# Optimization experiments

Hardware: AMD Instinct MI355X
Metric: run time of the kernel (lower is better)

Reference implementation:

```python
import jax, jax.numpy as jnp
import numpy as np

B, S, D_IN, D_OUT = 8, 2048, 4096, 4096
R, NUM_LABELERS = 32, 5
LORA_SCALING = 16 / 32  # lora_alpha / lora_r


def setup_inputs() -> dict:
    key = jax.random.key(0)
    k1, k2, k3, k4, k5, k6 = jax.random.split(key, 6)
    inp = {
        "input": jax.random.normal(k1, (B, S, D_IN), dtype=jnp.float32),
        "weight": jax.random.normal(k2, (D_OUT, D_IN), dtype=jnp.float32) * 0.02,
        "bias": jax.random.normal(k3, (D_OUT,), dtype=jnp.float32) * 0.02,
        "lora_A": jax.random.normal(k4, (NUM_LABELERS, D_IN, R), dtype=jnp.float32) * 0.02,
        "lora_B": jax.random.normal(k5, (D_OUT, R), dtype=jnp.float32) * 0.02,  # nn.Linear(r, out) weight
        "labeler_index": jax.random.randint(k6, (B,), 0, NUM_LABELERS, dtype=jnp.int64)
        if jax.config.jax_enable_x64 else jax.random.randint(k6, (B,), 0, NUM_LABELERS, dtype=jnp.int32),
    }
    return inp


def reference(input, weight, bias, lora_A, lora_B, labeler_index):
    # Base linear: F.linear(input, weight, bias) = input @ weight.T + bias
    base = jnp.einsum("bsi,oi->bso", input, weight) + bias
    # Gather per-labeler A matrices: [B, D_IN, R]
    labelers_A = lora_A[labeler_index]
    # Low-rank path: (x @ A_b) @ B.T, dropout is Identity (p=0)
    ax = jnp.einsum("bsi,bir->bsr", input, labelers_A)       # [B, S, R]
    delta = jnp.einsum("bsr,or->bso", ax, lora_B)            # [B, S, D_OUT]
    return base + delta * LORA_SCALING
```

## Files before the change

kernel.cpp:

```cpp
#include <hip/hip_runtime.h>
#include <hip/hip_bf16.h>


typedef __bf16 bf16_t;
typedef bf16_t bf16x4 __attribute__((ext_vector_type(4)));
typedef bf16_t bf16x8 __attribute__((ext_vector_type(8)));
typedef float f32x4 __attribute__((ext_vector_type(4)));

#define S_    2048
#define DIN   4096
#define DOUT  4096
#define R_    32
#define M_TOT 16384
#define KSPLIT 8

__device__ __forceinline__ void async_cp16(const bf16_t* g, bf16_t* l) {
  __builtin_amdgcn_global_load_lds((const __attribute__((address_space(1))) void*)g,
                                   (__attribute__((address_space(3))) void*)l,
                                   16, 0, 0);
}

__global__ void cast_f32_to_bf16(const float* __restrict__ src,
                                 bf16_t* __restrict__ dst, int n4) {
  int i = blockIdx.x * blockDim.x + threadIdx.x;
  if (i >= n4) return;
  f32x4 v = ((const f32x4*)src)[i];
  bf16x4 o = { (bf16_t)v[0], (bf16_t)v[1], (bf16_t)v[2], (bf16_t)v[3] };
  ((bf16x4*)dst)[i] = o;
}

__global__ __launch_bounds__(256) void transpose_loraA(
    const float* __restrict__ A, bf16_t* __restrict__ At) {
  __shared__ float tile[64][33];
  const int l = blockIdx.x / (DIN / 64);
  const int k0 = (blockIdx.x % (DIN / 64)) * 64;
  const int tid = threadIdx.x;
  {
    const int r = tid & 31, kb = tid >> 5;
#pragma unroll
    for (int p = 0; p < 8; ++p) {
      int k = p * 8 + kb;
      tile[k][r] = A[(size_t)l * DIN * R_ + (size_t)(k0 + k) * R_ + r];
    }
  }
  __syncthreads();
  {
    const int k = tid & 63, rb = tid >> 6;
#pragma unroll
    for (int p = 0; p < 8; ++p) {
      int r = p * 4 + rb;
      At[(size_t)l * R_ * DIN + (size_t)r * DIN + k0 + k] = (bf16_t)tile[k][r];
    }
  }
}

__global__ __launch_bounds__(256) void ax_partial(
    const bf16_t* __restrict__ Xb, const bf16_t* __restrict__ At,
    const int* __restrict__ lab_idx, float* __restrict__ axp) {
  __shared__ bf16_t As[128 * 64];
  __shared__ bf16_t Bs[32 * 64];
  const int tid = threadIdx.x, lane = tid & 63, wv = tid >> 6;
  const int m0 = blockIdx.x * 128;
  const int kbase = blockIdx.y * (DIN / KSPLIT);
  const int lab = lab_idx[m0 / S_];
  const bf16_t* Bsrc = At + (size_t)lab * R_ * DIN;

  f32x4 acc[2][2];
#pragma unroll
  for (int i = 0; i < 2; ++i)
#pragma unroll
    for (int j = 0; j < 2; ++j) acc[i][j] = (f32x4){0.f, 0.f, 0.f, 0.f};

  for (int kt = 0; kt < (DIN / KSPLIT) / 64; ++kt) {
    const int k0 = kbase + kt * 64;
    __syncthreads();
    {
      const int kk = (lane & 7) * 8;
#pragma unroll
      for (int j = 0; j < 4; ++j) {
        int row = j * 32 + wv * 8 + (lane >> 3);
        async_cp16(Xb + (size_t)(m0 + row) * DIN + k0 + kk,
                   As + j * 2048 + wv * 512);
      }
      int row = wv * 8 + (lane >> 3);
      async_cp16(Bsrc + (size_t)row * DIN + k0 + kk, Bs + wv * 512);
    }
    __syncthreads();
#pragma unroll
    for (int ks = 0; ks < 2; ++ks) {
      bf16x8 a[2], b[2];
#pragma unroll
      for (int mt = 0; mt < 2; ++mt)
        a[mt] = *(const bf16x8*)&As[(wv * 32 + mt * 16 + (lane & 15)) * 64 +
                                    ks * 32 + (lane >> 4) * 8];
#pragma unroll
      for (int nt = 0; nt < 2; ++nt)
        b[nt] = *(const bf16x8*)&Bs[(nt * 16 + (lane & 15)) * 64 +
                                    ks * 32 + (lane >> 4) * 8];
#pragma unroll
      for (int mt = 0; mt < 2; ++mt)
#pragma unroll
        for (int nt = 0; nt < 2; ++nt)
          acc[mt][nt] = __builtin_amdgcn_mfma_f32_16x16x32_bf16(
              a[mt], b[nt], acc[mt][nt], 0, 0, 0);
    }
  }
  float* dst = axp + (size_t)blockIdx.y * M_TOT * R_;
#pragma unroll
  for (int mt = 0; mt < 2; ++mt)
#pragma unroll
    for (int nt = 0; nt < 2; ++nt)
#pragma unroll
      for (int r = 0; r < 4; ++r) {
        int m = m0 + wv * 32 + mt * 16 + (lane >> 4) * 4 + r;
        int n = nt * 16 + (lane & 15);
        dst[(size_t)m * R_ + n] = acc[mt][nt][r];
      }
}

__global__ void ax_reduce(const float* __restrict__ axp,
                          bf16_t* __restrict__ axb, int n4) {
  int i = blockIdx.x * blockDim.x + threadIdx.x;
  if (i >= n4) return;
  f32x4 s = (f32x4){0.f, 0.f, 0.f, 0.f};
#pragma unroll
  for (int ks = 0; ks < KSPLIT; ++ks)
    s += ((const f32x4*)(axp + (size_t)ks * M_TOT * R_))[i];
  bf16x4 o = { (bf16_t)(0.5f * s[0]), (bf16_t)(0.5f * s[1]),
               (bf16_t)(0.5f * s[2]), (bf16_t)(0.5f * s[3]) };
  ((bf16x4*)axb)[i] = o;
}

__global__ __launch_bounds__(256) void main_gemm(
    const bf16_t* __restrict__ Xb, const bf16_t* __restrict__ Wb,
    const bf16_t* __restrict__ axb, const bf16_t* __restrict__ Bb,
    const float* __restrict__ bias, float* __restrict__ out) {
  __shared__ bf16_t As[128 * 32];
  __shared__ bf16_t Bs[128 * 32];
  const int tid = threadIdx.x, lane = tid & 63, wv = tid >> 6;
  const int wr = wv & 1, wc = wv >> 1;
  const int m0 = blockIdx.y * 128, n0 = blockIdx.x * 128;

  const int srow = wv * 16 + (lane >> 2);
  const int skk = (lane & 3) * 8;
  const bf16_t* pa0 = Xb + (size_t)(m0 + srow) * DIN + skk;
  const bf16_t* pa1 = pa0 + (size_t)64 * DIN;
  const bf16_t* pb0 = Wb + (size_t)(n0 + srow) * DIN + skk;
  const bf16_t* pb1 = pb0 + (size_t)64 * DIN;
  bf16_t* lA0 = As + wv * 512;
  bf16_t* lA1 = As + 2048 + wv * 512;
  bf16_t* lB0 = Bs + wv * 512;
  bf16_t* lB1 = Bs + 2048 + wv * 512;

  int offA[4], offB[4];
#pragma unroll
  for (int t = 0; t < 4; ++t) {
    offA[t] = (wr * 64 + t * 16 + (lane & 15)) * 32 + (lane >> 4) * 8;
    offB[t] = (wc * 64 + t * 16 + (lane & 15)) * 32 + (lane >> 4) * 8;
  }

  f32x4 acc[4][4];
#pragma unroll
  for (int i = 0; i < 4; ++i)
#pragma unroll
    for (int j = 0; j < 4; ++j) acc[i][j] = (f32x4){0.f, 0.f, 0.f, 0.f};

  for (int kt = 0; kt < 128; ++kt) {
    __syncthreads();
    async_cp16(pa0, lA0);
    async_cp16(pa1, lA1);
    async_cp16(pb0, lB0);
    async_cp16(pb1, lB1);
    pa0 += 32; pa1 += 32; pb0 += 32; pb1 += 32;
    __syncthreads();
    bf16x8 a[4], b[4];
#pragma unroll
    for (int t = 0; t < 4; ++t) {
      a[t] = *(const bf16x8*)&As[offA[t]];
      b[t] = *(const bf16x8*)&Bs[offB[t]];
    }
#pragma unroll
    for (int mt = 0; mt < 4; ++mt)
#pragma unroll
      for (int nt = 0; nt < 4; ++nt)
        acc[mt][nt] = __builtin_amdgcn_mfma_f32_16x16x32_bf16(
            a[mt], b[nt], acc[mt][nt], 0, 0, 0);
  }
  __syncthreads();
  async_cp16(axb + (size_t)(m0 + srow) * R_ + skk, lA0);
  async_cp16(axb + (size_t)(m0 + 64 + srow) * R_ + skk, lA1);
  async_cp16(Bb + (size_t)(n0 + srow) * R_ + skk, lB0);
  async_cp16(Bb + (size_t)(n0 + 64 + srow) * R_ + skk, lB1);
  __syncthreads();
  {
    bf16x8 a[4], b[4];
#pragma unroll
    for (int t = 0; t < 4; ++t) {
      a[t] = *(const bf16x8*)&As[offA[t]];
      b[t] = *(const bf16x8*)&Bs[offB[t]];
    }
#pragma unroll
    for (int mt = 0; mt < 4; ++mt)
#pragma unroll
      for (int nt = 0; nt < 4; ++nt)
        acc[mt][nt] = __builtin_amdgcn_mfma_f32_16x16x32_bf16(
            a[mt], b[nt], acc[mt][nt], 0, 0, 0);
  }
#pragma unroll
  for (int nt = 0; nt < 4; ++nt) {
    int n = n0 + wc * 64 + nt * 16 + (lane & 15);
    float bv = bias[n];
#pragma unroll
    for (int mt = 0; mt < 4; ++mt) {
      int m = m0 + wr * 64 + mt * 16 + (lane >> 4) * 4;
#pragma unroll
      for (int r = 0; r < 4; ++r)
        out[(size_t)(m + r) * DOUT + n] = acc[mt][nt][r] + bv;
    }
  }
}

extern "C" void kernel_launch(void* const* d_in, const int* in_sizes, int n_in,
                              void* d_out, int out_size, void* d_ws, size_t ws_size,
                              hipStream_t stream) {
  const float* X      = (const float*)d_in[0];
  const float* W      = (const float*)d_in[1];
  const float* bias   = (const float*)d_in[2];
  const float* lora_A = (const float*)d_in[3];
  const float* lora_B = (const float*)d_in[4];
  const int*   lab    = (const int*)d_in[5];
  float* out = (float*)d_out;

  char* ws = (char*)d_ws;
  bf16_t* Xb  = (bf16_t*)(ws);
  bf16_t* Wb  = (bf16_t*)(ws + 134217728UL);
  bf16_t* At  = (bf16_t*)(ws + 167772160UL);
  bf16_t* Bb  = (bf16_t*)(ws + 169082880UL);
  bf16_t* axb = (bf16_t*)(ws + 169345024UL);
  float*  axp = (float*)(ws + 170393600UL);

  cast_f32_to_bf16<<<65536, 256, 0, stream>>>(X, Xb, (M_TOT * DIN) / 4);
  cast_f32_to_bf16<<<16384, 256, 0, stream>>>(W, Wb, (DOUT * DIN) / 4);
  cast_f32_to_bf16<<<128, 256, 0, stream>>>(lora_B, Bb, (DOUT * R_) / 4);
  transpose_loraA<<<5 * (DIN / 64), 256, 0, stream>>>(lora_A, At);
  ax_partial<<<dim3(M_TOT / 128, KSPLIT), 256, 0, stream>>>(Xb, At, lab, axp);
  ax_reduce<<<(M_TOT * R_ / 4 + 255) / 256, 256, 0, stream>>>(
      axp, axb, M_TOT * R_ / 4);
  dim3 grid(DOUT / 128, M_TOT / 128);
  main_gemm<<<grid, 256, 0, stream>>>(Xb, Wb, axb, Bb, bias, out);
}
```

Before: 1.123 ms.

## Rewrite main GEMM with 256x256 tiles, double-buffered swizzled LDS and XCD grid remap

The main bf16 GEMM moves from 128x128 tiles with 256 threads and a load/sync/compute loop to 256x256 tiles with 512 threads. It double-buffers LDS and interleaves async global-to-LDS loads with MFMA phases using explicit barriers, waitcnt and setprio. It also XOR-swizzles the LDS layout to avoid bank conflicts and remaps block IDs for locality across XCDs. The aim is to hide memory latency and raise data reuse per tile, at the cost of many accumulator registers and about 128KB of LDS per block, plus fragile hand-written synchronisation.

```diff
diff --git a/kernel.cpp b/kernel.cpp
--- a/kernel.cpp
+++ b/kernel.cpp
@@ -131,91 +131,141 @@
   ((bf16x4*)axb)[i] = o;
 }
 
-__global__ __launch_bounds__(256) void main_gemm(
+__global__ __launch_bounds__(512, 2) void main_gemm(
     const bf16_t* __restrict__ Xb, const bf16_t* __restrict__ Wb,
     const bf16_t* __restrict__ axb, const bf16_t* __restrict__ Bb,
     const float* __restrict__ bias, float* __restrict__ out) {
-  __shared__ bf16_t As[128 * 32];
-  __shared__ bf16_t Bs[128 * 32];
+  __shared__ bf16_t lds[2][2][2][8192];
+  char* ldsb = (char*)&lds[0][0][0][0];
+
   const int tid = threadIdx.x, lane = tid & 63, wv = tid >> 6;
-  const int wr = wv & 1, wc = wv >> 1;
-  const int m0 = blockIdx.y * 128, n0 = blockIdx.x * 128;
-
-  const int srow = wv * 16 + (lane >> 2);
-  const int skk = (lane & 3) * 8;
-  const bf16_t* pa0 = Xb + (size_t)(m0 + srow) * DIN + skk;
-  const bf16_t* pa1 = pa0 + (size_t)64 * DIN;
-  const bf16_t* pb0 = Wb + (size_t)(n0 + srow) * DIN + skk;
-  const bf16_t* pb1 = pb0 + (size_t)64 * DIN;
-  bf16_t* lA0 = As + wv * 512;
-  bf16_t* lA1 = As + 2048 + wv * 512;
-  bf16_t* lB0 = Bs + wv * 512;
-  bf16_t* lB1 = Bs + 2048 + wv * 512;
-
-  int offA[4], offB[4];
-#pragma unroll
-  for (int t = 0; t < 4; ++t) {
-    offA[t] = (wr * 64 + t * 16 + (lane & 15)) * 32 + (lane >> 4) * 8;
-    offB[t] = (wc * 64 + t * 16 + (lane & 15)) * 32 + (lane >> 4) * 8;
-  }
-
-  f32x4 acc[4][4];
-#pragma unroll
-  for (int i = 0; i < 4; ++i)
+  const int wm = wv & 1, wn = wv >> 1;
+
+  const int swz = (blockIdx.x & 7) * 128 + (blockIdx.x >> 3);
+  const int m0 = (swz >> 4) * 256, n0 = (swz & 15) * 256;
+
+  const int rd_off = (lane & 15) * 64 + ((((lane >> 4) ^ (lane >> 1)) & 3) << 4);
+  const char* ldsA0 = ldsb + wm * 8192 + rd_off;
+  const char* ldsA1 = ldsA0 + 65536;
+  const char* ldsB0 = ldsb + 32768 + wn * 4096 + rd_off;
+  const char* ldsB1 = ldsB0 + 65536;
+
+  const int srow = lane >> 2;
+  const int scol = (((lane & 3) ^ (lane >> 3)) & 3) * 8;
+  const bf16_t* pA_w = Xb + (size_t)(m0 + wv * 16 + srow) * DIN + scol;
+  const bf16_t* pB_w = Wb + (size_t)(n0 + wv * 16 + srow) * DIN + scol;
+  char* lAw = ldsb + wv * 1024;
+  char* lBw = ldsb + 32768 + wv * 1024;
+
+  f32x4 acc[8][4];
+#pragma unroll
+  for (int i = 0; i < 8; ++i)
 #pragma unroll
     for (int j = 0; j < 4; ++j) acc[i][j] = (f32x4){0.f, 0.f, 0.f, 0.f};
 
-  for (int kt = 0; kt < 128; ++kt) {
-    __syncthreads();
-    async_cp16(pa0, lA0);
-    async_cp16(pa1, lA1);
-    async_cp16(pb0, lB0);
-    async_cp16(pb1, lB1);
-    pa0 += 32; pa1 += 32; pb0 += 32; pb1 += 32;
-    __syncthreads();
-    bf16x8 a[4], b[4];
-#pragma unroll
-    for (int t = 0; t < 4; ++t) {
-      a[t] = *(const bf16x8*)&As[offA[t]];
-      b[t] = *(const bf16x8*)&Bs[offB[t]];
-    }
-#pragma unroll
-    for (int mt = 0; mt < 4; ++mt)
-#pragma unroll
-      for (int nt = 0; nt < 4; ++nt)
-        acc[mt][nt] = __builtin_amdgcn_mfma_f32_16x16x32_bf16(
-            a[mt], b[nt], acc[mt][nt], 0, 0, 0);
-  }
-  __syncthreads();
-  async_cp16(axb + (size_t)(m0 + srow) * R_ + skk, lA0);
-  async_cp16(axb + (size_t)(m0 + 64 + srow) * R_ + skk, lA1);
-  async_cp16(Bb + (size_t)(n0 + srow) * R_ + skk, lB0);
-  async_cp16(Bb + (size_t)(n0 + 64 + srow) * R_ + skk, lB1);
-  __syncthreads();
+#define STAGE_A(buf, kh, st) do {                                        \
+    const bf16_t* g_ = pA_w + (st) * 64 + (kh) * 32;                     \
+    bf16_t* l_ = (bf16_t*)(lAw + (buf) * 65536 + (kh) * 16384);          \
+    async_cp16(g_, l_);                                                  \
+    async_cp16(g_ + 128 * DIN, l_ + 4096);                               \
+  } while (0)
+
+#define STAGE_B(buf, kh, st) do {                                        \
+    const bf16_t* g_ = pB_w + (st) * 64 + (kh) * 32;                     \
+    bf16_t* l_ = (bf16_t*)(lBw + (buf) * 65536 + (kh) * 16384);          \
+    async_cp16(g_, l_);                                                  \
+    async_cp16(g_ + 128 * DIN, l_ + 4096);                               \
+  } while (0)
+
+  bf16x8 bfr[4];
+
+#define PHASE(buf, ks, mh, LOADB, STAGE_STMT, VM) do {                   \
+    const char* pa_ = (buf) ? ldsA1 : ldsA0;                             \
+    const char* pb_ = (buf) ? ldsB1 : ldsB0;                             \
+    bf16x8 a_[4];                                                        \
+    _Pragma("unroll")                                                    \
+    for (int m_ = 0; m_ < 4; ++m_)                                       \
+      a_[m_] = *(const bf16x8*)(pa_ + (ks) * 16384 + ((mh) * 4 + m_) * 1024); \
+    if (LOADB) {                                                         \
+      _Pragma("unroll")                                                  \
+      for (int n_ = 0; n_ < 4; ++n_)                                     \
+        bfr[n_] = *(const bf16x8*)(pb_ + (ks) * 16384 + n_ * 1024);      \
+    }                                                                    \
+    STAGE_STMT;                                                          \
+    __builtin_amdgcn_s_barrier();                                        \
+    asm volatile("s_waitcnt lgkmcnt(0)" ::: "memory");                   \
+    __builtin_amdgcn_s_setprio(1);                                       \
+    _Pragma("unroll")                                                    \
+    for (int m_ = 0; m_ < 4; ++m_)                                       \
+      _Pragma("unroll")                                                  \
+      for (int n_ = 0; n_ < 4; ++n_)                                     \
+        acc[(mh) * 4 + m_][n_] = __builtin_amdgcn_mfma_f32_16x16x32_bf16( \
+            a_[m_], bfr[n_], acc[(mh) * 4 + m_][n_], 0, 0, 0);           \
+    __builtin_amdgcn_s_setprio(0);                                       \
+    VM;                                                                  \
+    __builtin_amdgcn_s_barrier();                                        \
+  } while (0)
+
+  STAGE_A(0, 0, 0); STAGE_B(0, 0, 0);
+  STAGE_A(0, 1, 0); STAGE_B(0, 1, 0);
+  STAGE_A(1, 0, 1); STAGE_B(1, 0, 1);
+  asm volatile("s_waitcnt vmcnt(4)" ::: "memory");
+  __builtin_amdgcn_s_barrier();
+
+  for (int i = 0; i < 32; ++i) {
+    const int st1 = 2 * i + 1;
+    const int st2 = (2 * i + 2 < 64) ? 2 * i + 2 : 63;
+    const int st3 = (2 * i + 3 < 64) ? 2 * i + 3 : 63;
+    PHASE(0, 0, 0, 1, STAGE_A(1, 1, st1), );
+    PHASE(0, 0, 1, 0, STAGE_B(1, 1, st1), );
+    PHASE(0, 1, 0, 1, STAGE_A(0, 0, st2), );
+    PHASE(0, 1, 1, 0, STAGE_B(0, 0, st2),
+          asm volatile("s_waitcnt vmcnt(4)" ::: "memory"));
+    PHASE(1, 0, 0, 1, STAGE_A(0, 1, st2), );
+    PHASE(1, 0, 1, 0, STAGE_B(0, 1, st2), );
+    PHASE(1, 1, 0, 1, STAGE_A(1, 0, st3), );
+    PHASE(1, 1, 1, 0, STAGE_B(1, 0, st3),
+          asm volatile("s_waitcnt vmcnt(4)" ::: "memory"));
+  }
+
   {
-    bf16x8 a[4], b[4];
-#pragma unroll
-    for (int t = 0; t < 4; ++t) {
-      a[t] = *(const bf16x8*)&As[offA[t]];
-      b[t] = *(const bf16x8*)&Bs[offB[t]];
-    }
-#pragma unroll
-    for (int mt = 0; mt < 4; ++mt)
-#pragma unroll
-      for (int nt = 0; nt < 4; ++nt)
-        acc[mt][nt] = __builtin_amdgcn_mfma_f32_16x16x32_bf16(
-            a[mt], b[nt], acc[mt][nt], 0, 0, 0);
-  }
-#pragma unroll
-  for (int nt = 0; nt < 4; ++nt) {
-    int n = n0 + wc * 64 + nt * 16 + (lane & 15);
-    float bv = bias[n];
-#pragma unroll
-    for (int mt = 0; mt < 4; ++mt) {
-      int m = m0 + wr * 64 + mt * 16 + (lane >> 4) * 4;
+    const bf16_t* gA = axb + (size_t)(m0 + wv * 16 + srow) * R_ + scol;
+    const bf16_t* gB = Bb + (size_t)(n0 + wv * 16 + srow) * R_ + scol;
+    bf16_t* lA = (bf16_t*)lAw;
+    bf16_t* lB = (bf16_t*)lBw;
+    async_cp16(gA, lA); async_cp16(gA + 128 * R_, lA + 4096);
+    async_cp16(gB, lB); async_cp16(gB + 128 * R_, lB + 4096);
+    asm volatile("s_waitcnt vmcnt(0)" ::: "memory");
+    __builtin_amdgcn_s_barrier();
+    bf16x8 a8[8];
+#pragma unroll
+    for (int m = 0; m < 8; ++m)
+      a8[m] = *(const bf16x8*)(ldsA0 + m * 1024);
+#pragma unroll
+    for (int n = 0; n < 4; ++n)
+      bfr[n] = *(const bf16x8*)(ldsB0 + n * 1024);
+    asm volatile("s_waitcnt lgkmcnt(0)" ::: "memory");
+#pragma unroll
+    for (int m = 0; m < 8; ++m)
+#pragma unroll
+      for (int n = 0; n < 4; ++n)
+        acc[m][n] = __builtin_amdgcn_mfma_f32_16x16x32_bf16(
+            a8[m], bfr[n], acc[m][n], 0, 0, 0);
+  }
+#undef PHASE
+#undef STAGE_A
+#undef STAGE_B
+
+#pragma unroll
+  for (int nf = 0; nf < 4; ++nf) {
+    const int n = n0 + wn * 64 + nf * 16 + (lane & 15);
+    const float bv = bias[n];
+#pragma unroll
+    for (int mf = 0; mf < 8; ++mf) {
+      const int m = m0 + wm * 128 + mf * 16 + (lane >> 4) * 4;
 #pragma unroll
       for (int r = 0; r < 4; ++r)
-        out[(size_t)(m + r) * DOUT + n] = acc[mt][nt][r] + bv;
+        out[(size_t)(m + r) * DOUT + n] = acc[mf][nf][r] + bv;
     }
   }
 }
@@ -246,6 +296,5 @@
   ax_partial<<<dim3(M_TOT / 128, KSPLIT), 256, 0, stream>>>(Xb, At, lab, axp);
   ax_reduce<<<(M_TOT * R_ / 4 + 255) / 256, 256, 0, stream>>>(
       axp, axb, M_TOT * R_ / 4);
-  dim3 grid(DOUT / 128, M_TOT / 128);
-  main_gemm<<<grid, 256, 0, stream>>>(Xb, Wb, axb, Bb, bias, out);
-}
+  main_gemm<<<1024, 512, 0, stream>>>(Xb, Wb, axb, Bb, bias, out);
+}
```

New measurement: 973.1 us. -13.4%, faster.
